# Kernel optimization log

Measured on AMD Instinct MI355X. Metric: run time of the kernel, lower is better.

The kernel has to match this reference:

```python
import jax, jax.numpy as jnp
import numpy as np

N_NODES = 100000
BASE_DIM = 128
E1 = 500000
E2 = 250000
N_TYPES = 4


def setup_inputs() -> dict:
    key = jax.random.key(0)
    ks = jax.random.split(key, 9)
    x = jax.random.normal(ks[0], (N_NODES, BASE_DIM), dtype=jnp.float32)
    # per-edge-type dense transforms (shape-1: d->d, shape-2: 2d->d)
    W1 = jax.random.normal(ks[1], (N_TYPES, BASE_DIM, BASE_DIM), dtype=jnp.float32) * 0.05
    W2 = jax.random.normal(ks[2], (N_TYPES, 2 * BASE_DIM, BASE_DIM), dtype=jnp.float32) * 0.05
    src1 = jax.random.randint(ks[3], (E1,), 0, N_NODES, dtype=jnp.int32)
    tgt1 = jax.random.randint(ks[4], (E1,), 0, N_NODES, dtype=jnp.int32)
    type1 = jax.random.randint(ks[5], (E1,), 0, N_TYPES, dtype=jnp.int32)
    src2 = jax.random.randint(ks[6], (2 * E2,), 0, N_NODES, dtype=jnp.int32)
    tgt2 = jax.random.randint(ks[7], (E2,), 0, N_NODES, dtype=jnp.int32)
    type2 = jax.random.randint(ks[8], (E2,), 0, N_TYPES, dtype=jnp.int32)
    return {"x": x, "W1": W1, "W2": W2, "src1": src1, "tgt1": tgt1,
            "type1": type1, "src2": src2, "tgt2": tgt2, "type2": type2}


def _gather_transform_scatter(x, W, src, tgt, etype, arity, n_nodes):
    # gather `arity` source nodes per hyperedge and concat features: (E, arity*d)
    d = x.shape[1]
    concat = x[src].reshape(-1, arity * d)
    # per-edge-type dense transform; small loop over fixed #types, masked accumulate
    acc = jnp.zeros((concat.shape[0], d), dtype=x.dtype)
    for t in range(W.shape[0]):
        acc = acc + jnp.where((etype == t)[:, None], concat @ W[t], 0.0)
    # scatter-add messages to target nodes
    return jax.ops.segment_sum(acc, tgt, num_segments=n_nodes)


def reference(x, W1, W2, src1, tgt1, type1, src2, tgt2, type2):
    n = x.shape[0]
    out = x
    out = out + _gather_transform_scatter(x, W1, src1, tgt1, type1, 1, n)
    out = out + _gather_transform_scatter(x, W2, src2, tgt2, type2, 2, n)
    return out
```

## Files before the change

kernel.cpp:

```cpp
#include <hip/hip_runtime.h>
#include <hip/hip_bf16.h>

#define D 128
#define EPB 32
#define NB 256

typedef __attribute__((ext_vector_type(8))) short bf16x8;
typedef __attribute__((ext_vector_type(4))) float f32x4;

__device__ inline unsigned short f2bf(float f) {
    union { float f; unsigned int u; } v;
    v.f = f;
    unsigned int u = v.u;
    unsigned int r = u + 0x7fffu + ((u >> 16) & 1u);
    return (unsigned short)(r >> 16);
}
__device__ inline float bf2f(unsigned short b) {
    union { unsigned int u; float f; } v;
    v.u = ((unsigned int)b) << 16;
    return v.f;
}
__device__ inline float bflo(unsigned u) { return bf2f((unsigned short)(u & 0xffff)); }
__device__ inline float bfhi(unsigned u) { return bf2f((unsigned short)(u >> 16)); }

__global__ __launch_bounds__(256) void copy_kernel(float* __restrict__ out,
                                                   const float* __restrict__ x,
                                                   int n_elems) {
    int n4 = n_elems >> 2;
    const float4* src = (const float4*)x;
    float4* dst = (float4*)out;
    for (int i = blockIdx.x * blockDim.x + threadIdx.x; i < n4;
         i += gridDim.x * blockDim.x)
        dst[i] = src[i];
}

__global__ __launch_bounds__(256) void conv_w(const float* __restrict__ W,
                                              unsigned short* __restrict__ Wt,
                                              int K) {
    __shared__ float tile[32][33];
    int k0 = blockIdx.x * 32, c0 = blockIdx.y * 32, t = blockIdx.z;
    int tr = threadIdx.x >> 5, tc = threadIdx.x & 31;
#pragma unroll
    for (int m = 0; m < 4; m++)
        tile[m * 8 + tr][tc] = W[((size_t)t * K + k0 + m * 8 + tr) * D + c0 + tc];
    __syncthreads();
#pragma unroll
    for (int m = 0; m < 4; m++)
        Wt[((size_t)t * D + c0 + m * 8 + tr) * K + k0 + tc] = f2bf(tile[tc][m * 8 + tr]);
}

__global__ __launch_bounds__(256) void hist_types(const int* __restrict__ type,
                                                  int n, int* __restrict__ hist) {
    __shared__ int h[4];
    if (threadIdx.x < 4) h[threadIdx.x] = 0;
    __syncthreads();
    for (int i = blockIdx.x * 256 + threadIdx.x; i < n; i += NB * 256)
        atomicAdd(&h[type[i]], 1);
    __syncthreads();
    if (threadIdx.x < 4) hist[blockIdx.x * 4 + threadIdx.x] = h[threadIdx.x];
}

__global__ void scan_offsets(int* __restrict__ meta,
                             const int* __restrict__ hist1, int* __restrict__ off1,
                             const int* __restrict__ hist2, int* __restrict__ off2) {
    int t = threadIdx.x;
    if (t < 4) {
        int s = 0;
        for (int b = 0; b < NB; b++) s += hist1[b * 4 + t];
        meta[t] = s;
    } else if (t < 8) {
        int tt = t - 4, s = 0;
        for (int b = 0; b < NB; b++) s += hist2[b * 4 + tt];
        meta[4 + tt] = s;
    }
    __syncthreads();
    if (t == 0) {
        int p = 0;
        for (int k = 0; k < 4; k++) {
            meta[8 + k] = p;
            p += ((meta[k] + EPB - 1) / EPB) * EPB;
        }
        meta[12] = p;
        p = 0;
        for (int k = 0; k < 4; k++) {
            meta[13 + k] = p;
            p += ((meta[4 + k] + EPB - 1) / EPB) * EPB;
        }
        meta[17] = p;
    }
    __syncthreads();
    if (t < 4) {
        int p = meta[8 + t];
        for (int b = 0; b < NB; b++) { off1[b * 4 + t] = p; p += hist1[b * 4 + t]; }
    } else if (t < 8) {
        int tt = t - 4;
        int p = meta[13 + tt];
        for (int b = 0; b < NB; b++) { off2[b * 4 + tt] = p; p += hist2[b * 4 + tt]; }
    }
}

__global__ __launch_bounds__(256) void write_sorted(const int* __restrict__ type,
                                                    int n,
                                                    const int* __restrict__ off,
                                                    int* __restrict__ sorted) {
    __shared__ int loff[4];
    if (threadIdx.x < 4) loff[threadIdx.x] = off[blockIdx.x * 4 + threadIdx.x];
    __syncthreads();
    for (int i = blockIdx.x * 256 + threadIdx.x; i < n; i += NB * 256) {
        int t = type[i];
        int pos = atomicAdd(&loff[t], 1);
        sorted[pos] = i;
    }
}

__global__ __launch_bounds__(256) void assign_rel(const int* __restrict__ tgt, int n,
                                                  int* __restrict__ cnt,
                                                  int* __restrict__ pos) {
    for (int i = blockIdx.x * blockDim.x + threadIdx.x; i < n;
         i += gridDim.x * blockDim.x)
        pos[i] = atomicAdd(&cnt[tgt[i]], 1);
}

__global__ __launch_bounds__(256) void scan_pass1(const int* __restrict__ cnt, int n,
                                                  int* __restrict__ base,
                                                  int* __restrict__ bsum) {
    __shared__ int s[256];
    int b = blockIdx.x, t = threadIdx.x;
    int i0 = b * 512 + 2 * t;
    int v0 = (i0 < n) ? cnt[i0] : 0;
    int v1 = (i0 + 1 < n) ? cnt[i0 + 1] : 0;
    s[t] = v0 + v1;
    __syncthreads();
    for (int off = 1; off < 256; off <<= 1) {
        int v = s[t];
        int u = (t >= off) ? s[t - off] : 0;
        __syncthreads();
        s[t] = v + u;
        __syncthreads();
    }
    int excl = (t > 0) ? s[t - 1] : 0;
    if (i0 < n) base[i0] = excl;
    if (i0 + 1 < n) base[i0 + 1] = excl + v0;
    if (t == 255) bsum[b] = s[255];
}

__global__ __launch_bounds__(256) void scan_pass2(int* __restrict__ bsum, int nb) {
    __shared__ int s[256];
    int t = threadIdx.x;
    int run = 0;
    for (int b0 = 0; b0 < nb; b0 += 256) {
        int v = (b0 + t < nb) ? bsum[b0 + t] : 0;
        s[t] = v;
        __syncthreads();
        for (int off = 1; off < 256; off <<= 1) {
            int a = s[t];
            int u = (t >= off) ? s[t - off] : 0;
            __syncthreads();
            s[t] = a + u;
            __syncthreads();
        }
        if (b0 + t < nb) bsum[b0 + t] = run + ((t > 0) ? s[t - 1] : 0);
        int tot = s[255];
        __syncthreads();
        run += tot;
    }
    if (t == 0) bsum[nb] = run;
}

__global__ __launch_bounds__(256) void scan_pass3(int* __restrict__ base,
                                                  const int* __restrict__ bsum, int n) {
    int i = blockIdx.x * 256 + threadIdx.x;
    if (i < n) base[i] += bsum[i >> 9];
    else if (i == n) base[n] = bsum[(n + 511) >> 9];
}

#define RMASK ((1 << 27) - 1)
__global__ __launch_bounds__(256) void write_rec1(
    const int* __restrict__ src, const int* __restrict__ tgt,
    const int* __restrict__ type, int n, const int* __restrict__ base,
    const int* __restrict__ pos, int* __restrict__ rec) {
    for (int i = blockIdx.x * blockDim.x + threadIdx.x; i < n;
         i += gridDim.x * blockDim.x)
        rec[base[tgt[i]] + pos[i]] = src[i] | (type[i] << 27);
}

__global__ __launch_bounds__(256) void write_rec2(
    const int* __restrict__ src2, const int* __restrict__ tgt,
    const int* __restrict__ type, int n, const int* __restrict__ base,
    const int* __restrict__ pos, int* __restrict__ reca, int* __restrict__ recb) {
    for (int i = blockIdx.x * blockDim.x + threadIdx.x; i < n;
         i += gridDim.x * blockDim.x) {
        int s = base[tgt[i]] + pos[i];
        reca[s] = src2[2 * i] | (type[i] << 27);
        recb[s] = src2[2 * i + 1];
    }
}

__global__ __launch_bounds__(256) void dense12(
    const float* __restrict__ x, const unsigned short* __restrict__ wt1,
    const unsigned short* __restrict__ wt2, unsigned short* __restrict__ tabs,
    int nn) {
    __shared__ uint4 As4[2048];
    char* As = (char*)As4;
    int tid = threadIdx.x;
    int m0 = blockIdx.x * 128;

    {
        int r = tid >> 1;
        int u0 = tid & 1;
        int node = m0 + r;
        bool ok = node < nn;
        const float4* srow = (const float4*)(x + (size_t)node * D);
#pragma unroll
        for (int q = 0; q < 16; q++) {
            int u = u0 + 2 * q;
            float4 v = make_float4(0.f, 0.f, 0.f, 0.f);
            if (ok) v = srow[u];
            uint2 p;
            p.x = (unsigned)f2bf(v.x) | ((unsigned)f2bf(v.y) << 16);
            p.y = (unsigned)f2bf(v.z) | ((unsigned)f2bf(v.w) << 16);
            int byte = ((((u >> 1) * 16) ^ ((r & 7) << 4)) + (u & 1) * 8);
            *(uint2*)(As + r * 256 + byte) = p;
        }
    }
    __syncthreads();

    int wave = tid >> 6, lane = tid & 63;
    int lrow = lane & 15, lgrp = lane >> 4;
    int r0 = wave * 32;

    bf16x8 a[2][4];
#pragma unroll
    for (int fr = 0; fr < 2; fr++)
#pragma unroll
        for (int kk = 0; kk < 4; kk++) {
            int rr = r0 + fr * 16 + lrow;
            a[fr][kk] = *(const bf16x8*)(As + rr * 256 +
                                         ((kk * 64 + lgrp * 16) ^ ((rr & 7) << 4)));
        }

    for (int g = 0; g < 12; g++) {
        int t = g & 3;
        const unsigned short* W;
        int K, koff;
        if (g < 4) { W = wt1 + (size_t)t * D * D; K = D; koff = 0; }
        else if (g < 8) { W = wt2 + (size_t)t * D * 2 * D; K = 2 * D; koff = 0; }
        else { W = wt2 + (size_t)t * D * 2 * D; K = 2 * D; koff = D; }
        unsigned short* tab = tabs + (size_t)g * nn * D;

        for (int cf = 0; cf < 4; cf++) {
            int c0 = cf * 32;
            bf16x8 b[2][4];
#pragma unroll
            for (int fc = 0; fc < 2; fc++)
#pragma unroll
                for (int kk = 0; kk < 4; kk++)
                    b[fc][kk] = *(const bf16x8*)(W + (size_t)(c0 + fc * 16 + lrow) * K +
                                                 koff + kk * 32 + lgrp * 8);
            f32x4 acc[2][2];
#pragma unroll
            for (int i = 0; i < 2; i++)
#pragma unroll
                for (int j = 0; j < 2; j++) acc[i][j] = (f32x4){0.f, 0.f, 0.f, 0.f};
#pragma unroll
            for (int kk = 0; kk < 4; kk++) {
                acc[0][0] = __builtin_amdgcn_mfma_f32_16x16x32_bf16(a[0][kk], b[0][kk], acc[0][0], 0, 0, 0);
                acc[1][0] = __builtin_amdgcn_mfma_f32_16x16x32_bf16(a[1][kk], b[0][kk], acc[1][0], 0, 0, 0);
                acc[0][1] = __builtin_amdgcn_mfma_f32_16x16x32_bf16(a[0][kk], b[1][kk], acc[0][1], 0, 0, 0);
                acc[1][1] = __builtin_amdgcn_mfma_f32_16x16x32_bf16(a[1][kk], b[1][kk], acc[1][1], 0, 0, 0);
            }
#pragma unroll
            for (int fr = 0; fr < 2; fr++)
#pragma unroll
                for (int reg = 0; reg < 4; reg++) {
                    int node = m0 + r0 + fr * 16 + lgrp * 4 + reg;
                    if (node < nn) {
#pragma unroll
                        for (int fc = 0; fc < 2; fc++)
                            tab[(size_t)node * D + c0 + fc * 16 + lrow] =
                                f2bf(acc[fr][fc][reg]);
                    }
                }
        }
    }
}

__global__ __launch_bounds__(256) void gather_fin(
    const float* __restrict__ x, const unsigned short* __restrict__ tabs,
    const int* __restrict__ base1, const int* __restrict__ rec1,
    const int* __restrict__ base2, const int* __restrict__ rec2a,
    const int* __restrict__ rec2b, float* __restrict__ out, int nn) {
    int wib = threadIdx.x >> 6, lane = threadIdx.x & 63;
    for (int v = blockIdx.x * 4 + wib; v < nn; v += gridDim.x * 4) {
        float2 xv = *(const float2*)(x + (size_t)v * D + lane * 2);
        float a0 = xv.x, a1 = xv.y;

        int b0 = base1[v], b1 = base1[v + 1];
        int i = b0;
        for (; i + 1 < b1; i += 2) {
            int r0 = rec1[i], r1 = rec1[i + 1];
            const unsigned short* p0 =
                tabs + ((size_t)(unsigned)(r0 >> 27) * nn + (r0 & RMASK)) * D;
            const unsigned short* p1 =
                tabs + ((size_t)(unsigned)(r1 >> 27) * nn + (r1 & RMASK)) * D;
            unsigned u0 = *(const unsigned*)(p0 + lane * 2);
            unsigned u1 = *(const unsigned*)(p1 + lane * 2);
            a0 += bflo(u0) + bflo(u1);
            a1 += bfhi(u0) + bfhi(u1);
        }
        if (i < b1) {
            int r0 = rec1[i];
            const unsigned short* p0 =
                tabs + ((size_t)(unsigned)(r0 >> 27) * nn + (r0 & RMASK)) * D;
            unsigned u0 = *(const unsigned*)(p0 + lane * 2);
            a0 += bflo(u0);
            a1 += bfhi(u0);
        }

        int c0 = base2[v], c1 = base2[v + 1];
        for (int j = c0; j < c1; j++) {
            int ra = rec2a[j], sb = rec2b[j];
            int t = (int)((unsigned)ra >> 27), sa = ra & RMASK;
            const unsigned short* pu = tabs + ((size_t)(4 + t) * nn + sa) * D;
            const unsigned short* pl = tabs + ((size_t)(8 + t) * nn + sb) * D;
            unsigned uu = *(const unsigned*)(pu + lane * 2);
            unsigned ul = *(const unsigned*)(pl + lane * 2);
            a0 += bflo(uu) + bflo(ul);
            a1 += bfhi(uu) + bfhi(ul);
        }
        *(float2*)(out + (size_t)v * D + lane * 2) = make_float2(a0, a1);
    }
}

__global__ __launch_bounds__(256) void edge1_msg(
    const float* __restrict__ x, const unsigned short* __restrict__ Wt1,
    const int* __restrict__ src, const int* __restrict__ tgt,
    const int* __restrict__ sorted, const int* __restrict__ meta,
    const int* __restrict__ basep, const int* __restrict__ pos,
    unsigned short* __restrict__ msg) {
    __shared__ uint4 As4[512];
    __shared__ int s_mrow[EPB];
    __shared__ int s_src[EPB];
    char* As = (char*)As4;

    int tid = threadIdx.x;
    int g0 = blockIdx.x * EPB;
    const int* pb = meta + 8;
    int t = 0;
#pragma unroll
    for (int k = 1; k < 4; k++)
        if (g0 >= pb[k]) t = k;
    const unsigned short* __restrict__ W = Wt1 + (size_t)t * D * D;

    if (tid < EPB) {
        int eid = sorted[g0 + tid];
        int sv = -1, mr = -1;
        if (eid >= 0) { sv = src[eid]; mr = basep[tgt[eid]] + pos[eid]; }
        s_src[tid] = sv;
        s_mrow[tid] = mr;
    }
    __syncthreads();
    {
        int r = tid >> 3, u0 = tid & 7;
        int sv = s_src[r];
        const float4* srow = (const float4*)(x + (size_t)sv * D);
#pragma unroll
        for (int q = 0; q < 4; q++) {
            int u = u0 + 8 * q;
            float4 v = make_float4(0.f, 0.f, 0.f, 0.f);
            if (sv >= 0) v = srow[u];
            uint2 p;
            p.x = (unsigned)f2bf(v.x) | ((unsigned)f2bf(v.y) << 16);
            p.y = (unsigned)f2bf(v.z) | ((unsigned)f2bf(v.w) << 16);
            int byte = ((((u >> 1) * 16) ^ ((r & 7) << 4)) + (u & 1) * 8);
            *(uint2*)(As + r * 256 + byte) = p;
        }
    }
    __syncthreads();

    int wave = tid >> 6, lane = tid & 63;
    int c0 = wave * 32;
    int lrow = lane & 15, lgrp = lane >> 4;

    bf16x8 b[2][4];
#pragma unroll
    for (int fc = 0; fc < 2; fc++)
#pragma unroll
        for (int kk = 0; kk < 4; kk++)
            b[fc][kk] = *(const bf16x8*)(W + (size_t)(c0 + fc * 16 + lrow) * D +
                                         kk * 32 + lgrp * 8);

    f32x4 acc[2][2];
#pragma unroll
    for (int i = 0; i < 2; i++)
#pragma unroll
        for (int j = 0; j < 2; j++) acc[i][j] = (f32x4){0.f, 0.f, 0.f, 0.f};

#pragma unroll
    for (int kk = 0; kk < 4; kk++) {
        bf16x8 a0, a1;
        {
            int r = lrow;
            a0 = *(const bf16x8*)(As + r * 256 + ((kk * 64 + lgrp * 16) ^ ((r & 7) << 4)));
        }
        {
            int r = 16 + lrow;
            a1 = *(const bf16x8*)(As + r * 256 + ((kk * 64 + lgrp * 16) ^ ((r & 7) << 4)));
        }
        acc[0][0] = __builtin_amdgcn_mfma_f32_16x16x32_bf16(a0, b[0][kk], acc[0][0], 0, 0, 0);
        acc[1][0] = __builtin_amdgcn_mfma_f32_16x16x32_bf16(a1, b[0][kk], acc[1][0], 0, 0, 0);
        acc[0][1] = __builtin_amdgcn_mfma_f32_16x16x32_bf16(a0, b[1][kk], acc[0][1], 0, 0, 0);
        acc[1][1] = __builtin_amdgcn_mfma_f32_16x16x32_bf16(a1, b[1][kk], acc[1][1], 0, 0, 0);
    }

#pragma unroll
    for (int fr = 0; fr < 2; fr++)
#pragma unroll
        for (int reg = 0; reg < 4; reg++) {
            int erow = fr * 16 + lgrp * 4 + reg;
            int mr = s_mrow[erow];
            if (mr >= 0) {
#pragma unroll
                for (int fc = 0; fc < 2; fc++)
                    msg[(size_t)mr * D + c0 + fc * 16 + lrow] = f2bf(acc[fr][fc][reg]);
            }
        }
}

__global__ __launch_bounds__(256) void edge2_msg(
    const float* __restrict__ x, const unsigned short* __restrict__ Wt2,
    const int* __restrict__ src2, const int* __restrict__ tgt,
    const int* __restrict__ sorted, const int* __restrict__ meta,
    const int* __restrict__ basep, const int* __restrict__ pos,
    unsigned short* __restrict__ msg) {
    __shared__ uint4 As4[1024];
    __shared__ int s_mrow[EPB];
    __shared__ int s_srcA[EPB];
    __shared__ int s_srcB[EPB];
    char* As = (char*)As4;

    int tid = threadIdx.x;
    int g0 = blockIdx.x * EPB;
    const int* pb = meta + 13;
    int t = 0;
#pragma unroll
    for (int k = 1; k < 4; k++)
        if (g0 >= pb[k]) t = k;
    const unsigned short* __restrict__ W = Wt2 + (size_t)t * D * 2 * D;

    if (tid < EPB) {
        int eid = sorted[g0 + tid];
        int sa = -1, sb = -1, mr = -1;
        if (eid >= 0) {
            sa = src2[2 * eid];
            sb = src2[2 * eid + 1];
            mr = basep[tgt[eid]] + pos[eid];
        }
        s_srcA[tid] = sa;
        s_srcB[tid] = sb;
        s_mrow[tid] = mr;
    }
    __syncthreads();
    {
        int r = tid >> 3, u0 = tid & 7;
        int sa = s_srcA[r], sb = s_srcB[r];
        const float4* rowA = (const float4*)(x + (size_t)sa * D);
        const float4* rowB = (const float4*)(x + (size_t)sb * D);
#pragma unroll
        for (int q = 0; q < 8; q++) {
            int u = u0 + 8 * q;
            float4 v = make_float4(0.f, 0.f, 0.f, 0.f);
            if (sa >= 0) v = (u < 32) ? rowA[u] : rowB[u - 32];
            uint2 p;
            p.x = (unsigned)f2bf(v.x) | ((unsigned)f2bf(v.y) << 16);
            p.y = (unsigned)f2bf(v.z) | ((unsigned)f2bf(v.w) << 16);
            int byte = ((((u >> 1) * 16) ^ ((r & 7) << 4)) + (u & 1) * 8);
            *(uint2*)(As + r * 512 + byte) = p;
        }
    }
    __syncthreads();

    int wave = tid >> 6, lane = tid & 63;
    int c0 = wave * 32;
    int lrow = lane & 15, lgrp = lane >> 4;

    f32x4 acc[2][2];
#pragma unroll
    for (int i = 0; i < 2; i++)
#pragma unroll
        for (int j = 0; j < 2; j++) acc[i][j] = (f32x4){0.f, 0.f, 0.f, 0.f};

#pragma unroll
    for (int kk = 0; kk < 8; kk++) {
        bf16x8 b0 = *(const bf16x8*)(W + (size_t)(c0 + lrow) * 2 * D + kk * 32 + lgrp * 8);
        bf16x8 b1 = *(const bf16x8*)(W + (size_t)(c0 + 16 + lrow) * 2 * D + kk * 32 + lgrp * 8);
        bf16x8 a0, a1;
        {
            int r = lrow;
            a0 = *(const bf16x8*)(As + r * 512 + ((kk * 64 + lgrp * 16) ^ ((r & 7) << 4)));
        }
        {
            int r = 16 + lrow;
            a1 = *(const bf16x8*)(As + r * 512 + ((kk * 64 + lgrp * 16) ^ ((r & 7) << 4)));
        }
        acc[0][0] = __builtin_amdgcn_mfma_f32_16x16x32_bf16(a0, b0, acc[0][0], 0, 0, 0);
        acc[1][0] = __builtin_amdgcn_mfma_f32_16x16x32_bf16(a1, b0, acc[1][0], 0, 0, 0);
        acc[0][1] = __builtin_amdgcn_mfma_f32_16x16x32_bf16(a0, b1, acc[0][1], 0, 0, 0);
        acc[1][1] = __builtin_amdgcn_mfma_f32_16x16x32_bf16(a1, b1, acc[1][1], 0, 0, 0);
    }

#pragma unroll
    for (int fr = 0; fr < 2; fr++)
#pragma unroll
        for (int reg = 0; reg < 4; reg++) {
            int erow = fr * 16 + lgrp * 4 + reg;
            int mr = s_mrow[erow];
            if (mr >= 0) {
#pragma unroll
                for (int fc = 0; fc < 2; fc++)
                    msg[(size_t)mr * D + c0 + fc * 16 + lrow] = f2bf(acc[fr][fc][reg]);
            }
        }
}

__global__ __launch_bounds__(256) void finalize(
    const float* __restrict__ x, const unsigned short* __restrict__ msg,
    const int* __restrict__ basep, float* __restrict__ out, int nn) {
    int wib = threadIdx.x >> 6, lane = threadIdx.x & 63;
    for (int v = blockIdx.x * 4 + wib; v < nn; v += gridDim.x * 4) {
        int b0 = basep[v], b1 = basep[v + 1];
        float2 xv = *(const float2*)(x + (size_t)v * D + lane * 2);
        float a0 = xv.x, a1 = xv.y;
        for (int i = b0; i < b1; i++) {
            unsigned u = *(const unsigned*)(msg + (size_t)i * D + lane * 2);
            a0 += bflo(u);
            a1 += bfhi(u);
        }
        *(float2*)(out + (size_t)v * D + lane * 2) = make_float2(a0, a1);
    }
}

__global__ __launch_bounds__(256) void e1_simple(
    const float* __restrict__ x, const float* __restrict__ W1,
    const int* __restrict__ src, const int* __restrict__ tgt,
    const int* __restrict__ type, float* __restrict__ out, int n) {
    int lane = threadIdx.x & 63;
    int wid = (blockIdx.x * blockDim.x + threadIdx.x) >> 6;
    int nw = (gridDim.x * blockDim.x) >> 6;
    for (int e = wid; e < n; e += nw) {
        const float* W = W1 + (size_t)type[e] * D * D;
        const float* xr = x + (size_t)src[e] * D;
        float a0 = 0.f, a1 = 0.f;
        for (int i = 0; i < D; i++) {
            float xv = xr[i];
            a0 = fmaf(xv, W[i * D + lane], a0);
            a1 = fmaf(xv, W[i * D + 64 + lane], a1);
        }
        atomicAdd(&out[(size_t)tgt[e] * D + lane], a0);
        atomicAdd(&out[(size_t)tgt[e] * D + 64 + lane], a1);
    }
}

__global__ __launch_bounds__(256) void e2_simple(
    const float* __restrict__ x, const float* __restrict__ W2,
    const int* __restrict__ src2, const int* __restrict__ tgt,
    const int* __restrict__ type, float* __restrict__ out, int n) {
    int lane = threadIdx.x & 63;
    int wid = (blockIdx.x * blockDim.x + threadIdx.x) >> 6;
    int nw = (gridDim.x * blockDim.x) >> 6;
    for (int e = wid; e < n; e += nw) {
        const float* W = W2 + (size_t)type[e] * 2 * D * D;
        const float* xrA = x + (size_t)src2[2 * e] * D;
        const float* xrB = x + (size_t)src2[2 * e + 1] * D;
        float a0 = 0.f, a1 = 0.f;
        for (int i = 0; i < 2 * D; i++) {
            float xv = (i < D) ? xrA[i] : xrB[i - D];
            a0 = fmaf(xv, W[i * D + lane], a0);
            a1 = fmaf(xv, W[i * D + 64 + lane], a1);
        }
        atomicAdd(&out[(size_t)tgt[e] * D + lane], a0);
        atomicAdd(&out[(size_t)tgt[e] * D + 64 + lane], a1);
    }
}

extern "C" void kernel_launch(void* const* d_in, const int* in_sizes, int n_in,
                              void* d_out, int out_size, void* d_ws, size_t ws_size,
                              hipStream_t stream) {
    const float* x = (const float*)d_in[0];
    const float* W1 = (const float*)d_in[1];
    const float* W2 = (const float*)d_in[2];
    const int* src1 = (const int*)d_in[3];
    const int* tgt1 = (const int*)d_in[4];
    const int* type1 = (const int*)d_in[5];
    const int* src2 = (const int*)d_in[6];
    const int* tgt2 = (const int*)d_in[7];
    const int* type2 = (const int*)d_in[8];
    float* out = (float*)d_out;

    int nn = in_sizes[0] / D;
    int E1c = in_sizes[3];
    int E2c = in_sizes[7];

    int nb_scan = (nn + 511) / 512;
    size_t w1_elems = (size_t)4 * D * D;
    size_t w2_elems = (size_t)4 * D * 2 * D;
    size_t wt_bytes = (w1_elems + w2_elems) * 2;

    size_t o_cnt1 = 0;
    size_t o_cnt2 = o_cnt1 + nn;
    size_t o_base1 = o_cnt2 + nn;
    size_t o_base2 = o_base1 + nn + 1;
    size_t o_bsum1 = o_base2 + nn + 1;
    size_t o_bsum2 = o_bsum1 + nb_scan + 1;
    size_t o_pos1d = o_bsum2 + nb_scan + 1;
    size_t o_pos2d = o_pos1d + E1c;
    size_t o_rec1 = o_pos2d + E2c;
    size_t o_rec2a = o_rec1 + E1c;
    size_t o_rec2b = o_rec2a + E2c;
    size_t ints_dense = o_rec2b + E2c;
    size_t wtd_off = (ints_dense * 4 + 255) & ~(size_t)255;
    size_t tab_off = (wtd_off + wt_bytes + 255) & ~(size_t)255;
    size_t tab_bytes = (size_t)12 * nn * D * 2;
    size_t need_dense = tab_off + tab_bytes;

    int grid1 = (E1c + 4 * (EPB - 1) + EPB - 1) / EPB;
    int grid2 = (E2c + 4 * (EPB - 1) + EPB - 1) / EPB;
    int cap1 = grid1 * EPB;
    int cap2 = grid2 * EPB;
    size_t o_meta = 0;
    size_t o_hist1 = o_meta + 32;
    size_t o_off1 = o_hist1 + (size_t)NB * 4;
    size_t o_hist2 = o_off1 + (size_t)NB * 4;
    size_t o_off2 = o_hist2 + (size_t)NB * 4;
    size_t o_sorted1 = o_off2 + (size_t)NB * 4;
    size_t o_sorted2 = o_sorted1 + cap1;
    size_t o_pos1 = o_sorted2 + cap2;
    size_t o_pos2 = o_pos1 + E1c;
    size_t o_cnt = o_pos2 + E2c;
    size_t o_base = o_cnt + nn;
    size_t o_bsum = o_base + nn + 1;
    size_t ints_full = o_bsum + nb_scan + 1;
    size_t ints_r3 = o_pos1;
    size_t wb_full = (ints_full * 4 + 255) & ~(size_t)255;
    size_t wb_r3 = (ints_r3 * 4 + 255) & ~(size_t)255;
    size_t msg_off = (wb_full + wt_bytes + 255) & ~(size_t)255;
    size_t msg_bytes = (size_t)(E1c + E2c) * D * 2;
    size_t need_full = msg_off + msg_bytes;
    size_t need_r3 = wb_r3 + wt_bytes;

    if (ws_size >= need_dense && nn < (1 << 27)) {
        int* wsI = (int*)d_ws;
        int* cnt1 = wsI + o_cnt1;
        int* cnt2 = wsI + o_cnt2;
        int* base1 = wsI + o_base1;
        int* base2 = wsI + o_base2;
        int* bsum1 = wsI + o_bsum1;
        int* bsum2 = wsI + o_bsum2;
        int* pos1 = wsI + o_pos1d;
        int* pos2 = wsI + o_pos2d;
        int* rec1 = wsI + o_rec1;
        int* rec2a = wsI + o_rec2a;
        int* rec2b = wsI + o_rec2b;
        unsigned short* wt1 = (unsigned short*)((char*)d_ws + wtd_off);
        unsigned short* wt2 = wt1 + w1_elems;
        unsigned short* tabs = (unsigned short*)((char*)d_ws + tab_off);

        hipMemsetAsync(cnt1, 0, (size_t)8 * nn, stream);

        conv_w<<<dim3(4, 4, 4), 256, 0, stream>>>(W1, wt1, D);
        conv_w<<<dim3(8, 4, 4), 256, 0, stream>>>(W2, wt2, 2 * D);

        assign_rel<<<2048, 256, 0, stream>>>(tgt1, E1c, cnt1, pos1);
        assign_rel<<<2048, 256, 0, stream>>>(tgt2, E2c, cnt2, pos2);

        scan_pass1<<<nb_scan, 256, 0, stream>>>(cnt1, nn, base1, bsum1);
        scan_pass2<<<1, 256, 0, stream>>>(bsum1, nb_scan);
        scan_pass3<<<(nn + 1 + 255) / 256, 256, 0, stream>>>(base1, bsum1, nn);
        scan_pass1<<<nb_scan, 256, 0, stream>>>(cnt2, nn, base2, bsum2);
        scan_pass2<<<1, 256, 0, stream>>>(bsum2, nb_scan);
        scan_pass3<<<(nn + 1 + 255) / 256, 256, 0, stream>>>(base2, bsum2, nn);

        write_rec1<<<2048, 256, 0, stream>>>(src1, tgt1, type1, E1c, base1, pos1, rec1);
        write_rec2<<<2048, 256, 0, stream>>>(src2, tgt2, type2, E2c, base2, pos2,
                                             rec2a, rec2b);

        dense12<<<(nn + 127) / 128, 256, 0, stream>>>(x, wt1, wt2, tabs, nn);

        gather_fin<<<(nn + 3) / 4, 256, 0, stream>>>(x, tabs, base1, rec1, base2,
                                                     rec2a, rec2b, out, nn);
    } else if (ws_size >= need_full) {
        int* wsI = (int*)d_ws;
        int* meta = wsI + o_meta;
        int* hist1 = wsI + o_hist1;
        int* off1 = wsI + o_off1;
        int* hist2 = wsI + o_hist2;
        int* off2 = wsI + o_off2;
        int* sorted1 = wsI + o_sorted1;
        int* sorted2 = wsI + o_sorted2;
        int* pos1 = wsI + o_pos1;
        int* pos2 = wsI + o_pos2;
        int* cnt = wsI + o_cnt;
        int* basep = wsI + o_base;
        int* bsum = wsI + o_bsum;
        unsigned short* wt1 = (unsigned short*)((char*)d_ws + wb_full);
        unsigned short* wt2 = wt1 + w1_elems;
        unsigned short* msg = (unsigned short*)((char*)d_ws + msg_off);

        hipMemsetAsync(sorted1, 0xFF, (size_t)4 * (cap1 + cap2), stream);
        hipMemsetAsync(cnt, 0, (size_t)4 * nn, stream);

        conv_w<<<dim3(4, 4, 4), 256, 0, stream>>>(W1, wt1, D);
        conv_w<<<dim3(8, 4, 4), 256, 0, stream>>>(W2, wt2, 2 * D);

        hist_types<<<NB, 256, 0, stream>>>(type1, E1c, hist1);
        hist_types<<<NB, 256, 0, stream>>>(type2, E2c, hist2);
        scan_offsets<<<1, 64, 0, stream>>>(meta, hist1, off1, hist2, off2);
        write_sorted<<<NB, 256, 0, stream>>>(type1, E1c, off1, sorted1);
        write_sorted<<<NB, 256, 0, stream>>>(type2, E2c, off2, sorted2);

        assign_rel<<<2048, 256, 0, stream>>>(tgt1, E1c, cnt, pos1);
        assign_rel<<<2048, 256, 0, stream>>>(tgt2, E2c, cnt, pos2);
        scan_pass1<<<nb_scan, 256, 0, stream>>>(cnt, nn, basep, bsum);
        scan_pass2<<<1, 256, 0, stream>>>(bsum, nb_scan);
        scan_pass3<<<(nn + 1 + 255) / 256, 256, 0, stream>>>(basep, bsum, nn);

        edge1_msg<<<grid1, 256, 0, stream>>>(x, wt1, src1, tgt1, sorted1, meta,
                                             basep, pos1, msg);
        edge2_msg<<<grid2, 256, 0, stream>>>(x, wt2, src2, tgt2, sorted2, meta,
                                             basep, pos2, msg);
        finalize<<<(nn + 3) / 4, 256, 0, stream>>>(x, msg, basep, out, nn);
    } else {
        copy_kernel<<<2048, 256, 0, stream>>>(out, x, nn * D);
        e1_simple<<<2048, 256, 0, stream>>>(x, W1, src1, tgt1, type1, out, E1c);
        e2_simple<<<2048, 256, 0, stream>>>(x, W2, src2, tgt2, type2, out, E2c);
    }
}
```

Baseline: 345.2 us.

## Split dense tables into two stages and stage tile stores through shared memory

```diff
diff --git a/kernel.cpp b/kernel.cpp
--- a/kernel.cpp
+++ b/kernel.cpp
@@ -4,6 +4,7 @@
 #define D 128
 #define EPB 32
 #define NB 256
+#define RMASK ((1 << 27) - 1)
 
 typedef __attribute__((ext_vector_type(8))) short bf16x8;
 typedef __attribute__((ext_vector_type(4))) float f32x4;
@@ -174,7 +175,6 @@
     else if (i == n) base[n] = bsum[(n + 511) >> 9];
 }
 
-#define RMASK ((1 << 27) - 1)
 __global__ __launch_bounds__(256) void write_rec1(
     const int* __restrict__ src, const int* __restrict__ tgt,
     const int* __restrict__ type, int n, const int* __restrict__ base,
@@ -196,18 +196,18 @@
     }
 }
 
-__global__ __launch_bounds__(256) void dense12(
-    const float* __restrict__ x, const unsigned short* __restrict__ wt1,
-    const unsigned short* __restrict__ wt2, unsigned short* __restrict__ tabs,
-    int nn) {
+__global__ __launch_bounds__(256) void dense_tab(
+    const float* __restrict__ x, const unsigned short* __restrict__ wt,
+    unsigned short* __restrict__ tabs, int nn, int stage) {
     __shared__ uint4 As4[2048];
+    __shared__ unsigned short Cs[128 * 128];
     char* As = (char*)As4;
+    char* Csb = (char*)Cs;
     int tid = threadIdx.x;
     int m0 = blockIdx.x * 128;
 
     {
-        int r = tid >> 1;
-        int u0 = tid & 1;
+        int r = tid >> 1, u0 = tid & 1;
         int node = m0 + r;
         bool ok = node < nn;
         const float4* srow = (const float4*)(x + (size_t)node * D);
@@ -239,13 +239,12 @@
                                          ((kk * 64 + lgrp * 16) ^ ((rr & 7) << 4)));
         }
 
-    for (int g = 0; g < 12; g++) {
+    int ng = stage ? 8 : 4;
+    int K = stage ? 2 * D : D;
+    for (int g = 0; g < ng; g++) {
         int t = g & 3;
-        const unsigned short* W;
-        int K, koff;
-        if (g < 4) { W = wt1 + (size_t)t * D * D; K = D; koff = 0; }
-        else if (g < 8) { W = wt2 + (size_t)t * D * 2 * D; K = 2 * D; koff = 0; }
-        else { W = wt2 + (size_t)t * D * 2 * D; K = 2 * D; koff = D; }
+        int koff = stage ? ((g >> 2) * D) : 0;
+        const unsigned short* W = wt + (size_t)t * D * K;
         unsigned short* tab = tabs + (size_t)g * nn * D;
 
         for (int cf = 0; cf < 4; cf++) {
@@ -273,36 +272,45 @@
             for (int fr = 0; fr < 2; fr++)
 #pragma unroll
                 for (int reg = 0; reg < 4; reg++) {
-                    int node = m0 + r0 + fr * 16 + lgrp * 4 + reg;
-                    if (node < nn) {
-#pragma unroll
-                        for (int fc = 0; fc < 2; fc++)
-                            tab[(size_t)node * D + c0 + fc * 16 + lrow] =
-                                f2bf(acc[fr][fc][reg]);
+                    int row = r0 + fr * 16 + lgrp * 4 + reg;
+#pragma unroll
+                    for (int fc = 0; fc < 2; fc++) {
+                        int col = c0 + fc * 16 + lrow;
+                        *(unsigned short*)(Csb + row * 256 +
+                                           ((col * 2) ^ ((row & 7) << 4))) =
+                            f2bf(acc[fr][fc][reg]);
                     }
                 }
         }
-    }
-}
-
-__global__ __launch_bounds__(256) void gather_fin(
+        __syncthreads();
+#pragma unroll
+        for (int it = 0; it < 8; it++) {
+            int flat = tid + it * 256;
+            int row = flat >> 4, j = flat & 15;
+            if (m0 + row < nn)
+                *(uint4*)(tab + ((size_t)(m0 + row)) * D + j * 8) =
+                    *(const uint4*)(Csb + row * 256 + ((j ^ (row & 7)) * 16));
+        }
+        __syncthreads();
+    }
+}
+
+__global__ __launch_bounds__(256) void gather1(
     const float* __restrict__ x, const unsigned short* __restrict__ tabs,
     const int* __restrict__ base1, const int* __restrict__ rec1,
-    const int* __restrict__ base2, const int* __restrict__ rec2a,
-    const int* __restrict__ rec2b, float* __restrict__ out, int nn) {
+    float* __restrict__ out, int nn) {
     int wib = threadIdx.x >> 6, lane = threadIdx.x & 63;
     for (int v = blockIdx.x * 4 + wib; v < nn; v += gridDim.x * 4) {
         float2 xv = *(const float2*)(x + (size_t)v * D + lane * 2);
         float a0 = xv.x, a1 = xv.y;
-
         int b0 = base1[v], b1 = base1[v + 1];
         int i = b0;
         for (; i + 1 < b1; i += 2) {
             int r0 = rec1[i], r1 = rec1[i + 1];
             const unsigned short* p0 =
-                tabs + ((size_t)(unsigned)(r0 >> 27) * nn + (r0 & RMASK)) * D;
+                tabs + ((size_t)((unsigned)r0 >> 27) * nn + (r0 & RMASK)) * D;
             const unsigned short* p1 =
-                tabs + ((size_t)(unsigned)(r1 >> 27) * nn + (r1 & RMASK)) * D;
+                tabs + ((size_t)((unsigned)r1 >> 27) * nn + (r1 & RMASK)) * D;
             unsigned u0 = *(const unsigned*)(p0 + lane * 2);
             unsigned u1 = *(const unsigned*)(p1 + lane * 2);
             a0 += bflo(u0) + bflo(u1);
@@ -311,18 +319,30 @@
         if (i < b1) {
             int r0 = rec1[i];
             const unsigned short* p0 =
-                tabs + ((size_t)(unsigned)(r0 >> 27) * nn + (r0 & RMASK)) * D;
+                tabs + ((size_t)((unsigned)r0 >> 27) * nn + (r0 & RMASK)) * D;
             unsigned u0 = *(const unsigned*)(p0 + lane * 2);
             a0 += bflo(u0);
             a1 += bfhi(u0);
         }
-
+        *(float2*)(out + (size_t)v * D + lane * 2) = make_float2(a0, a1);
+    }
+}
+
+__global__ __launch_bounds__(256) void gather2(
+    const unsigned short* __restrict__ tabs,
+    const int* __restrict__ base2, const int* __restrict__ rec2a,
+    const int* __restrict__ rec2b, float* __restrict__ out, int nn) {
+    int wib = threadIdx.x >> 6, lane = threadIdx.x & 63;
+    for (int v = blockIdx.x * 4 + wib; v < nn; v += gridDim.x * 4) {
         int c0 = base2[v], c1 = base2[v + 1];
+        if (c0 == c1) continue;
+        float2 ov = *(const float2*)(out + (size_t)v * D + lane * 2);
+        float a0 = ov.x, a1 = ov.y;
         for (int j = c0; j < c1; j++) {
             int ra = rec2a[j], sb = rec2b[j];
             int t = (int)((unsigned)ra >> 27), sa = ra & RMASK;
-            const unsigned short* pu = tabs + ((size_t)(4 + t) * nn + sa) * D;
-            const unsigned short* pl = tabs + ((size_t)(8 + t) * nn + sb) * D;
+            const unsigned short* pu = tabs + ((size_t)t * nn + sa) * D;
+            const unsigned short* pl = tabs + ((size_t)(4 + t) * nn + sb) * D;
             unsigned uu = *(const unsigned*)(pu + lane * 2);
             unsigned ul = *(const unsigned*)(pl + lane * 2);
             a0 += bflo(uu) + bflo(ul);
@@ -620,7 +640,7 @@
     size_t ints_dense = o_rec2b + E2c;
     size_t wtd_off = (ints_dense * 4 + 255) & ~(size_t)255;
     size_t tab_off = (wtd_off + wt_bytes + 255) & ~(size_t)255;
-    size_t tab_bytes = (size_t)12 * nn * D * 2;
+    size_t tab_bytes = (size_t)8 * nn * D * 2;
     size_t need_dense = tab_off + tab_bytes;
 
     int grid1 = (E1c + 4 * (EPB - 1) + EPB - 1) / EPB;
@@ -640,13 +660,10 @@
     size_t o_base = o_cnt + nn;
     size_t o_bsum = o_base + nn + 1;
     size_t ints_full = o_bsum + nb_scan + 1;
-    size_t ints_r3 = o_pos1;
     size_t wb_full = (ints_full * 4 + 255) & ~(size_t)255;
-    size_t wb_r3 = (ints_r3 * 4 + 255) & ~(size_t)255;
     size_t msg_off = (wb_full + wt_bytes + 255) & ~(size_t)255;
     size_t msg_bytes = (size_t)(E1c + E2c) * D * 2;
     size_t need_full = msg_off + msg_bytes;
-    size_t need_r3 = wb_r3 + wt_bytes;
 
     if (ws_size >= need_dense && nn < (1 << 27)) {
         int* wsI = (int*)d_ws;
@@ -684,10 +701,11 @@
         write_rec2<<<2048, 256, 0, stream>>>(src2, tgt2, type2, E2c, base2, pos2,
                                              rec2a, rec2b);
 
-        dense12<<<(nn + 127) / 128, 256, 0, stream>>>(x, wt1, wt2, tabs, nn);
-
-        gather_fin<<<(nn + 3) / 4, 256, 0, stream>>>(x, tabs, base1, rec1, base2,
-                                                     rec2a, rec2b, out, nn);
+        int gblk = (nn + 127) / 128;
+        dense_tab<<<gblk, 256, 0, stream>>>(x, wt1, tabs, nn, 0);
+        gather1<<<(nn + 3) / 4, 256, 0, stream>>>(x, tabs, base1, rec1, out, nn);
+        dense_tab<<<gblk, 256, 0, stream>>>(x, wt2, tabs, nn, 1);
+        gather2<<<(nn + 3) / 4, 256, 0, stream>>>(tabs, base2, rec2a, rec2b, out, nn);
     } else if (ws_size >= need_full) {
         int* wsI = (int*)d_ws;
         int* meta = wsI + o_meta;
```

New measurement: 401.2 us. +16.2%, slower.
